# Kernel tuning notes

Hardware: AMD Instinct MI355X
Metric: run time of the kernel (lower is better)

Reference implementation:

```python
import jax, jax.numpy as jnp
import numpy as np

EPS = 1e-8

def _ternary(w):
    # BitNet b1.58-style ternary weight quantization with per-matrix absmean scale.
    # STE: forward uses quantized weights, gradient flows through identity.
    s = jnp.mean(jnp.abs(w), axis=(-2, -1), keepdims=True) + EPS
    wq = jnp.clip(jnp.round(w / s), -1.0, 1.0) * s
    return w + jax.lax.stop_gradient(wq - w)

def setup_inputs() -> dict:
    key = jax.random.key(0)
    ks = jax.random.split(key, 8)
    d_model, d_register, n_phases, n_registers, d_align = 2048, 256, 3, 3, 512
    B, L = 4, 8192
    reg_real_dim = 2 * d_register * n_registers  # 1536
    def w(k, shape, fan_in):
        return jax.random.normal(k, shape, jnp.float32) * (1.0 / np.sqrt(fan_in))
    return {
        "delta": jax.random.normal(ks[0], (B, L, d_model), jnp.float32),
        # complex registers as real (n_registers, d_register, 2), last dim [real, imag]
        "registers": jax.random.normal(ks[1], (n_registers, d_register, 2), jnp.float32),
        "pa_w": w(ks[2], (n_phases, d_align, reg_real_dim), reg_real_dim),
        "pd_w": w(ks[3], (n_phases, d_align, d_model), d_model),
        "temperature": jnp.ones((n_phases,), jnp.float32),
        "learned_bias": jnp.zeros((n_phases,), jnp.float32),
        "wr_w": w(ks[4], (n_phases * n_registers, d_register, d_model), d_model),
        "wi_w": w(ks[5], (n_phases * n_registers, d_register, d_model), d_model),
        "wg_w": w(ks[6], (n_phases * n_registers, 1, d_model), d_model),
        "wg_b": jnp.zeros((n_phases * n_registers, 1), jnp.float32),
        "phase_idx": 1,
    }

def reference(delta, registers, pa_w, pd_w, temperature, learned_bias,
              wr_w, wi_w, wg_w, wg_b, phase_idx):
    n_registers = registers.shape[0]
    # _interleave_complex: view_as_real gives [r0,i0,r1,i1,...] per register, concat over regs
    reg_flat = registers.reshape(-1)                       # (n_registers*d_register*2,)
    reg_dir = reg_flat / (jnp.linalg.norm(reg_flat) + EPS)
    summary = delta.mean(axis=(0, 1))                      # (d_model,)
    delta_dir = summary / (jnp.linalg.norm(summary) + EPS)
    reg_proj = _ternary(pa_w[phase_idx]) @ reg_dir         # (d_align,)
    delta_proj = _ternary(pd_w[phase_idx]) @ delta_dir     # (d_align,)
    alignment = jnp.sum(reg_proj * delta_proj)
    gate = jax.nn.sigmoid(alignment * temperature[phase_idx] + learned_bias[phase_idx])
    gated_delta = gate * delta                             # (B, L, d_model)
    sl = slice(phase_idx * n_registers, (phase_idx + 1) * n_registers)
    wg = jax.nn.sigmoid(jnp.einsum('rod,d->ro', wg_w[sl], summary) + wg_b[sl])  # (R,1)
    upd_r = jnp.einsum('rkd,d->rk', _ternary(wr_w[sl]), summary)  # (R, d_register)
    upd_i = jnp.einsum('rkd,d->rk', _ternary(wi_w[sl]), summary)
    upd = jnp.stack([upd_r, upd_i], axis=-1)               # (R, d_register, 2)
    updated_registers = registers + wg[..., None] * upd
    return gated_delta, updated_registers, gate, wg[:, 0]
```

## Files before the change

### kernel.cpp

```cpp
#include <hip/hip_runtime.h>
#include <math.h>

typedef float f32x4 __attribute__((ext_vector_type(4)));

#define D_MODEL   2048
#define N_ROWS    32768
#define D_ALIGN   512
#define D_REG     256
#define N_REG     3
#define REG_FLAT  1536
#define EPSF      1e-8f

#define PA_N   (D_ALIGN * REG_FLAT)
#define PD_N   (D_ALIGN * D_MODEL)
#define W_N    (D_REG * D_MODEL)

#define OUT_REGS  ((size_t)N_ROWS * D_MODEL)
#define OUT_GATE  (OUT_REGS + REG_FLAT)
#define OUT_WG    (OUT_GATE + 1)

#define WS_SUMS      0
#define WS_ABSP      2048
#define WS_REGPROJ   2304
#define WS_DELTAPROJ 2816
#define WS_UPD       3328
#define WS_WG        4864
#define WS_PART      8192
#define NBY          512
#define WS_REQ_BYTES ((size_t)(WS_PART + NBY * D_MODEL) * sizeof(float))

#define TOTAL_ROWS    2563

__device__ __forceinline__ float bfly(float v) {
    #pragma unroll
    for (int o = 32; o > 0; o >>= 1) v += __shfl_xor(v, o, 64);
    return v;
}

__global__ __launch_bounds__(256) void k_stage1(const float* __restrict__ delta,
                                                const float* __restrict__ pa,
                                                const float* __restrict__ pd,
                                                const float* __restrict__ wr,
                                                const float* __restrict__ wi,
                                                const int* __restrict__ pidx,
                                                float* __restrict__ ws,
                                                int use_part) {
    const int b = blockIdx.x, t = threadIdx.x;
    if (b < NBY) {
        const f32x4* p = (const f32x4*)(delta + (size_t)b * 64 * D_MODEL);
        f32x4 a0 = {0.f, 0.f, 0.f, 0.f};
        f32x4 a1 = {0.f, 0.f, 0.f, 0.f};
        #pragma unroll 8
        for (int r = 0; r < 64; ++r) {
            a0 += p[r * 512 + t];
            a1 += p[r * 512 + t + 256];
        }
        if (use_part) {
            f32x4* part = (f32x4*)(ws + WS_PART);
            part[(size_t)b * 512 + t]       = a0;
            part[(size_t)b * 512 + t + 256] = a1;
        } else {
            atomicAdd(&ws[WS_SUMS + t * 4 + 0], a0.x);
            atomicAdd(&ws[WS_SUMS + t * 4 + 1], a0.y);
            atomicAdd(&ws[WS_SUMS + t * 4 + 2], a0.z);
            atomicAdd(&ws[WS_SUMS + t * 4 + 3], a0.w);
            atomicAdd(&ws[WS_SUMS + (t + 256) * 4 + 0], a1.x);
            atomicAdd(&ws[WS_SUMS + (t + 256) * 4 + 1], a1.y);
            atomicAdd(&ws[WS_SUMS + (t + 256) * 4 + 2], a1.z);
            atomicAdd(&ws[WS_SUMS + (t + 256) * 4 + 3], a1.w);
        }
    } else {
        const int idx = b - NBY;
        const int m = idx >> 5, chunk = idx & 31;
        const int pp = *pidx;
        const float* base; int n4;
        if (m == 0)      { base = pa + (size_t)pp * PA_N;                n4 = PA_N / 4; }
        else if (m == 1) { base = pd + (size_t)pp * PD_N;                n4 = PD_N / 4; }
        else if (m < 5)  { base = wr + (size_t)(pp * 3 + (m - 2)) * W_N; n4 = W_N / 4; }
        else             { base = wi + (size_t)(pp * 3 + (m - 5)) * W_N; n4 = W_N / 4; }
        const int per = n4 / 32;
        const int s = chunk * per, e = s + per;
        float acc = 0.f;
        for (int i = s + t; i < e; i += 256) {
            f32x4 v = __builtin_nontemporal_load(&((const f32x4*)base)[i]);
            acc += fabsf(v.x) + fabsf(v.y) + fabsf(v.z) + fabsf(v.w);
        }
        acc = bfly(acc);
        __shared__ float sh[4];
        if ((t & 63) == 0) sh[t >> 6] = acc;
        __syncthreads();
        if (t == 0) ws[WS_ABSP + idx] = sh[0] + sh[1] + sh[2] + sh[3];
    }
}

__global__ __launch_bounds__(256) void k_reduce(float* __restrict__ ws) {
    const int col = blockIdx.x * 256 + threadIdx.x;
    const float* part = ws + WS_PART;
    float acc = 0.f;
    for (int p = 0; p < NBY; ++p)
        acc += __builtin_nontemporal_load(&part[(size_t)p * D_MODEL + col]);
    ws[WS_SUMS + col] = acc;
}

__global__ __launch_bounds__(256) void k_matvec(const float* __restrict__ regs,
                                                const float* __restrict__ pa,
                                                const float* __restrict__ pd,
                                                const float* __restrict__ wr,
                                                const float* __restrict__ wi,
                                                const float* __restrict__ wgw,
                                                const float* __restrict__ wgb,
                                                const int* __restrict__ pidx,
                                                float* __restrict__ ws) {
    const int wid = threadIdx.x >> 6, lane = threadIdx.x & 63;
    const int row = blockIdx.x * 4 + wid;
    if (row >= TOTAL_ROWS) return;
    const int p = *pidx;

    const float* w; const float* x; int n4; int outIdx;
    float s = 0.f, post, bias = 0.f;
    bool tern = true;

    if (row < 512) {
        w = pa + (size_t)p * PA_N + (size_t)row * REG_FLAT;
        x = regs; n4 = REG_FLAT / 4;
        float a = (lane < 32) ? ws[WS_ABSP + lane] : 0.f;
        s = bfly(a) / (float)PA_N + EPSF;
        float q = 0.f;
        for (int i = lane; i < REG_FLAT / 4; i += 64) {
            f32x4 v = ((const f32x4*)regs)[i];
            q += v.x * v.x + v.y * v.y + v.z * v.z + v.w * v.w;
        }
        post = s / (sqrtf(bfly(q)) + EPSF);
        outIdx = WS_REGPROJ + row;
    } else if (row < 1024) {
        const int o = row - 512;
        w = pd + (size_t)p * PD_N + (size_t)o * D_MODEL;
        x = ws + WS_SUMS; n4 = D_MODEL / 4;
        float a = (lane < 32) ? ws[WS_ABSP + 32 + lane] : 0.f;
        s = bfly(a) / (float)PD_N + EPSF;
        float q = 0.f;
        for (int i = lane; i < D_MODEL / 4; i += 64) {
            f32x4 v = ((const f32x4*)(ws + WS_SUMS))[i];
            q += v.x * v.x + v.y * v.y + v.z * v.z + v.w * v.w;
        }
        post = s / (sqrtf(bfly(q)) + (float)N_ROWS * EPSF);
        outIdx = WS_DELTAPROJ + o;
    } else if (row < 2560) {
        const int t = row - 1024;
        const int half = t >= 768 ? 1 : 0;
        const int tt = t - half * 768;
        const int r = tt >> 8;
        const int m = 2 + half * 3 + r;
        w = (half ? wi : wr) + (size_t)(p * 3 + r) * W_N + (size_t)(tt & 255) * D_MODEL;
        x = ws + WS_SUMS; n4 = D_MODEL / 4;
        float a = (lane < 32) ? ws[WS_ABSP + m * 32 + lane] : 0.f;
        s = bfly(a) / (float)W_N + EPSF;
        post = s / (float)N_ROWS;
        outIdx = WS_UPD + t;
    } else {
        const int i = row - 2560;
        const int mm = p * 3 + i;
        w = wgw + (size_t)mm * D_MODEL;
        x = ws + WS_SUMS; n4 = D_MODEL / 4;
        tern = false;
        post = 1.f / (float)N_ROWS;
        bias = wgb[mm];
        outIdx = WS_WG + i;
    }

    float acc = 0.f;
    if (tern) {
        const float inv_s = 1.0f / s;
        for (int i = lane; i < n4; i += 64) {
            f32x4 wv = __builtin_nontemporal_load(&((const f32x4*)w)[i]);
            f32x4 xv = ((const f32x4*)x)[i];
            float q0 = fmaxf(-1.f, fminf(1.f, rintf(wv.x * inv_s)));
            float q1 = fmaxf(-1.f, fminf(1.f, rintf(wv.y * inv_s)));
            float q2 = fmaxf(-1.f, fminf(1.f, rintf(wv.z * inv_s)));
            float q3 = fmaxf(-1.f, fminf(1.f, rintf(wv.w * inv_s)));
            acc += q0 * xv.x + q1 * xv.y + q2 * xv.z + q3 * xv.w;
        }
    } else {
        for (int i = lane; i < n4; i += 64) {
            f32x4 wv = __builtin_nontemporal_load(&((const f32x4*)w)[i]);
            f32x4 xv = ((const f32x4*)x)[i];
            acc += wv.x * xv.x + wv.y * xv.y + wv.z * xv.z + wv.w * xv.w;
        }
    }
    acc = bfly(acc);
    if (lane == 0) ws[outIdx] = acc * post + bias;
}

__global__ __launch_bounds__(256) void k_scale(const f32x4* __restrict__ in,
                                               f32x4* __restrict__ out4,
                                               const float* __restrict__ ws,
                                               const float* __restrict__ regs,
                                               const float* __restrict__ temp,
                                               const float* __restrict__ lbias,
                                               const int* __restrict__ pidx,
                                               float* __restrict__ out) {
    const int tid = threadIdx.x;
    float a = 0.f;
    for (int i = tid; i < D_ALIGN; i += 256)
        a += ws[WS_REGPROJ + i] * ws[WS_DELTAPROJ + i];
    a = bfly(a);
    __shared__ float sh[4];
    if ((tid & 63) == 0) sh[tid >> 6] = a;
    __syncthreads();
    const int p = *pidx;
    const float align = sh[0] + sh[1] + sh[2] + sh[3];
    const float g = 1.f / (1.f + expf(-(align * temp[p] + lbias[p])));

    if (blockIdx.x == 0) {
        __shared__ float wg_s[N_REG];
        if (tid == 0) out[OUT_GATE] = g;
        if (tid < N_REG) {
            float v = 1.f / (1.f + expf(-ws[WS_WG + tid]));
            wg_s[tid] = v;
            out[OUT_WG + tid] = v;
        }
        __syncthreads();
        for (int t = tid; t < REG_FLAT; t += 256) {
            const int rk = t >> 1, c = t & 1;
            float u = ws[WS_UPD + c * 768 + rk];
            out[OUT_REGS + t] = regs[t] + wg_s[rk >> 8] * u;
        }
    }

    const size_t stride = (size_t)gridDim.x * 256;
    const size_t linear = (size_t)blockIdx.x * 256 + tid;
    #pragma unroll 4
    for (int j = 0; j < 32; ++j) {
        const size_t i = linear + (size_t)j * stride;
        f32x4 v = in[i];
        v *= g;
        __builtin_nontemporal_store(v, &out4[i]);
    }
}

extern "C" void kernel_launch(void* const* d_in, const int* in_sizes, int n_in,
                              void* d_out, int out_size, void* d_ws, size_t ws_size,
                              hipStream_t stream) {
    (void)in_sizes; (void)n_in; (void)out_size;
    const float* delta = (const float*)d_in[0];
    const float* regs  = (const float*)d_in[1];
    const float* pa    = (const float*)d_in[2];
    const float* pd    = (const float*)d_in[3];
    const float* temp  = (const float*)d_in[4];
    const float* lbias = (const float*)d_in[5];
    const float* wr    = (const float*)d_in[6];
    const float* wi    = (const float*)d_in[7];
    const float* wgw   = (const float*)d_in[8];
    const float* wgb   = (const float*)d_in[9];
    const int*   pidx  = (const int*)d_in[10];
    float* out = (float*)d_out;
    float* ws  = (float*)d_ws;

    const int use_part = (ws_size >= WS_REQ_BYTES) ? 1 : 0;
    if (!use_part)
        hipMemsetAsync(d_ws, 0, D_MODEL * sizeof(float), stream);

    k_stage1<<<NBY + 256, 256, 0, stream>>>(delta, pa, pd, wr, wi, pidx, ws, use_part);
    if (use_part)
        k_reduce<<<D_MODEL / 256, 256, 0, stream>>>(ws);
    k_matvec<<<(TOTAL_ROWS + 3) / 4, 256, 0, stream>>>(regs, pa, pd, wr, wi,
                                                       wgw, wgb, pidx, ws);
    k_scale<<<2048, 256, 0, stream>>>((const f32x4*)delta, (f32x4*)d_out, ws,
                                      regs, temp, lbias, pidx, out);
}
```

Baseline: 180.4 us.

## Tune cache hints, split reduce across blocks, add independent accumulators

Delta column-sum loads become nontemporal with two independent accumulator pairs, while the weight abs-sum loads drop the nontemporal hint. The partial-sum reduce now runs as an 8x8 grid, each block summing 64 partials and atomically adding into sums that stage1 zeroes first. The scale kernel uses nontemporal loads and a deeper unroll. The aim is more memory-level parallelism and less serialized reduction, at the cost of float atomics that make the summation order nondeterministic.

```diff
diff --git a/kernel.cpp b/kernel.cpp
--- a/kernel.cpp
+++ b/kernel.cpp
@@ -48,13 +48,18 @@
     const int b = blockIdx.x, t = threadIdx.x;
     if (b < NBY) {
         const f32x4* p = (const f32x4*)(delta + (size_t)b * 64 * D_MODEL);
-        f32x4 a0 = {0.f, 0.f, 0.f, 0.f};
-        f32x4 a1 = {0.f, 0.f, 0.f, 0.f};
+        f32x4 a0  = {0.f, 0.f, 0.f, 0.f};
+        f32x4 a0b = {0.f, 0.f, 0.f, 0.f};
+        f32x4 a1  = {0.f, 0.f, 0.f, 0.f};
+        f32x4 a1b = {0.f, 0.f, 0.f, 0.f};
         #pragma unroll 8
-        for (int r = 0; r < 64; ++r) {
-            a0 += p[r * 512 + t];
-            a1 += p[r * 512 + t + 256];
-        }
+        for (int r = 0; r < 64; r += 2) {
+            a0  += __builtin_nontemporal_load(&p[r * 512 + t]);
+            a1  += __builtin_nontemporal_load(&p[r * 512 + t + 256]);
+            a0b += __builtin_nontemporal_load(&p[(r + 1) * 512 + t]);
+            a1b += __builtin_nontemporal_load(&p[(r + 1) * 512 + t + 256]);
+        }
+        a0 += a0b; a1 += a1b;
         if (use_part) {
             f32x4* part = (f32x4*)(ws + WS_PART);
             part[(size_t)b * 512 + t]       = a0;
@@ -71,6 +76,9 @@
         }
     } else {
         const int idx = b - NBY;
+        if (use_part && idx == 0) {
+            for (int i = t; i < D_MODEL; i += 256) ws[WS_SUMS + i] = 0.f;
+        }
         const int m = idx >> 5, chunk = idx & 31;
         const int pp = *pidx;
         const float* base; int n4;
@@ -82,7 +90,7 @@
         const int s = chunk * per, e = s + per;
         float acc = 0.f;
         for (int i = s + t; i < e; i += 256) {
-            f32x4 v = __builtin_nontemporal_load(&((const f32x4*)base)[i]);
+            f32x4 v = ((const f32x4*)base)[i];
             acc += fabsf(v.x) + fabsf(v.y) + fabsf(v.z) + fabsf(v.w);
         }
         acc = bfly(acc);
@@ -95,11 +103,16 @@
 
 __global__ __launch_bounds__(256) void k_reduce(float* __restrict__ ws) {
     const int col = blockIdx.x * 256 + threadIdx.x;
-    const float* part = ws + WS_PART;
-    float acc = 0.f;
-    for (int p = 0; p < NBY; ++p)
-        acc += __builtin_nontemporal_load(&part[(size_t)p * D_MODEL + col]);
-    ws[WS_SUMS + col] = acc;
+    const float* part = ws + WS_PART + (size_t)blockIdx.y * 64 * D_MODEL;
+    float a0 = 0.f, a1 = 0.f, a2 = 0.f, a3 = 0.f;
+    #pragma unroll 8
+    for (int p = 0; p < 64; p += 4) {
+        a0 += part[(size_t)(p + 0) * D_MODEL + col];
+        a1 += part[(size_t)(p + 1) * D_MODEL + col];
+        a2 += part[(size_t)(p + 2) * D_MODEL + col];
+        a3 += part[(size_t)(p + 3) * D_MODEL + col];
+    }
+    atomicAdd(&ws[WS_SUMS + col], (a0 + a1) + (a2 + a3));
 }
 
 __global__ __launch_bounds__(256) void k_matvec(const float* __restrict__ regs,
@@ -229,10 +242,10 @@
 
     const size_t stride = (size_t)gridDim.x * 256;
     const size_t linear = (size_t)blockIdx.x * 256 + tid;
-    #pragma unroll 4
+    #pragma unroll 8
     for (int j = 0; j < 32; ++j) {
         const size_t i = linear + (size_t)j * stride;
-        f32x4 v = in[i];
+        f32x4 v = __builtin_nontemporal_load(&in[i]);
         v *= g;
         __builtin_nontemporal_store(v, &out4[i]);
     }
@@ -262,7 +275,7 @@
 
     k_stage1<<<NBY + 256, 256, 0, stream>>>(delta, pa, pd, wr, wi, pidx, ws, use_part);
     if (use_part)
-        k_reduce<<<D_MODEL / 256, 256, 0, stream>>>(ws);
+        k_reduce<<<dim3(8, 8), 256, 0, stream>>>(ws);
     k_matvec<<<(TOTAL_ROWS + 3) / 4, 256, 0, stream>>>(regs, pa, pd, wr, wi,
                                                        wgw, wgb, pidx, ws);
     k_scale<<<2048, 256, 0, stream>>>((const f32x4*)delta, (f32x4*)d_out, ws,
```

New measurement: 198.1 us. 9.8% more time.
